# Kernel tuning notes

Measured on AMD Instinct MI355X. Metric: run time of the kernel, lower is better.

## Reference

```python
import jax, jax.numpy as jnp
import numpy as np

NUM_HEADS = 12


def setup_inputs() -> dict:
    key = jax.random.key(0)
    k1, k2, k3, k4 = jax.random.split(key, 4)
    B, N, C = 8, 1024, 768
    x = jax.random.normal(k1, (B, N, C), dtype=jnp.float32)
    # nn.Linear(dim, 3*dim, bias=False): weight applied as x @ W, shape [C, 3C]
    w_qkv = jax.random.normal(k2, (C, 3 * C), dtype=jnp.float32) * (C ** -0.5)
    # nn.Linear(dim, dim) with bias
    w_proj = jax.random.normal(k3, (C, C), dtype=jnp.float32) * (C ** -0.5)
    b_proj = jax.random.normal(k4, (C,), dtype=jnp.float32) * 0.01
    return {"x": x, "w_qkv": w_qkv, "w_proj": w_proj, "b_proj": b_proj, "H": 32, "W": 32}


def reference(x, w_qkv, w_proj, b_proj, H, W):
    B, N, C = x.shape
    nh = NUM_HEADS
    hd = C // nh
    scale = hd ** -0.5
    qkv = (x @ w_qkv).reshape(B, N, 3, nh, hd)
    q, k, v = jnp.moveaxis(qkv, 2, 0)  # each [B, N, nh, hd]
    attn = jnp.einsum("bnhd,bmhd->bhnm", q, k) * scale  # [B, nh, N, N]
    attn = jax.nn.softmax(attn, axis=-1)
    out = jnp.einsum("bhnm,bmhd->bnhd", attn, v).reshape(B, N, C)
    return out @ w_proj + b_proj
```

## Files before the change

kernel.cpp:

```cpp
#include <hip/hip_runtime.h>

typedef __bf16 bf16x8 __attribute__((ext_vector_type(8)));
typedef float f32x4 __attribute__((ext_vector_type(4)));
typedef unsigned short u16;
typedef unsigned int u32;
typedef u16 u16x4 __attribute__((ext_vector_type(4)));

__device__ __forceinline__ u16 f2bf(float f) {
    union { float f; u32 u; } x{f};
    u32 r = x.u + 0x7FFFu + ((x.u >> 16) & 1u);
    return (u16)(r >> 16);
}

__device__ __forceinline__ float ex2(float x) {
#if __has_builtin(__builtin_amdgcn_exp2f)
    return __builtin_amdgcn_exp2f(x);
#else
    return __expf(x * 0.6931471805599453f);
#endif
}

#define GLD16(g, l)                                                            \
    __builtin_amdgcn_global_load_lds(                                          \
        (const __attribute__((address_space(1))) u32*)(g),                     \
        (__attribute__((address_space(3))) u32*)(l), 16, 0, 0)

__global__ void convert_bf16(const float* __restrict__ src, u16* __restrict__ dst, int n4) {
    int i = blockIdx.x * blockDim.x + threadIdx.x;
    if (i < n4) {
        float4 f = *(const float4*)(src + (size_t)i * 4);
        u16x4 u = { f2bf(f.x), f2bf(f.y), f2bf(f.z), f2bf(f.w) };
        *(u16x4*)(dst + (size_t)i * 4) = u;
    }
}

__global__ void transpose_conv(const float* __restrict__ src, u16* __restrict__ dst, int R, int C) {
    __shared__ u16 tile[32][33];
    int bx = blockIdx.x * 32;
    int by = blockIdx.y * 32;
    int x = threadIdx.x, y = threadIdx.y;
    #pragma unroll
    for (int i = 0; i < 32; i += 8)
        tile[y + i][x] = f2bf(src[(size_t)(by + y + i) * C + bx + x]);
    __syncthreads();
    #pragma unroll
    for (int i = 0; i < 32; i += 8)
        dst[(size_t)(bx + y + i) * R + by + x] = tile[x][y + i];
}

__global__ void transpose_v(const u16* __restrict__ qkv, u16* __restrict__ Vt) {
    __shared__ u16 tile[32][33];
    int nb = blockIdx.x * 32, db = blockIdx.y * 32, bh = blockIdx.z;
    int b = bh / 12, h = bh % 12;
    int x = threadIdx.x, y = threadIdx.y;
    #pragma unroll
    for (int i = 0; i < 32; i += 8)
        tile[y + i][x] = qkv[(size_t)(b * 1024 + nb + y + i) * 2304 + 1536 + h * 64 + db + x];
    __syncthreads();
    #pragma unroll
    for (int i = 0; i < 32; i += 8)
        Vt[((size_t)bh * 64 + db + y + i) * 1024 + nb + x] = tile[x][y + i];
}

#define BK 32
template <bool WRITE_BF16, bool ADD_BIAS>
__global__ __launch_bounds__(256) void gemm_bt(
    const u16* __restrict__ A,
    const u16* __restrict__ Bt,
    void* __restrict__ Cp,
    const float* __restrict__ bias,
    int M, int N, int K, int qcols, float qscale)
{
    __shared__ __align__(16) u16 As[128 * BK];
    __shared__ __align__(16) u16 Bs[128 * BK];

    int tid = threadIdx.x;
    int wave = tid >> 6, lane = tid & 63;
    int quad = lane >> 4, l16 = lane & 15;
    int wm = (wave >> 1) * 64, wn = (wave & 1) * 64;
    int bm = blockIdx.y * 128, bn = blockIdx.x * 128;

    f32x4 acc[4][4] = {};

    int srow = lane >> 2;
    int scg = (lane & 3) * 8;
    const u16* Aptr = A + (size_t)(bm + wave * 32 + srow) * K + scg;
    const u16* Bptr = Bt + (size_t)(bn + wave * 32 + srow) * K + scg;
    u16* AsW0 = &As[(wave * 32) * BK];
    u16* AsW1 = &As[(wave * 32 + 16) * BK];
    u16* BsW0 = &Bs[(wave * 32) * BK];
    u16* BsW1 = &Bs[(wave * 32 + 16) * BK];
    const size_t rstepA = (size_t)16 * K;

    for (int k0 = 0; k0 < K; k0 += BK) {
        GLD16(Aptr + k0,          AsW0);
        GLD16(Aptr + k0 + rstepA, AsW1);
        GLD16(Bptr + k0,          BsW0);
        GLD16(Bptr + k0 + rstepA, BsW1);
        __syncthreads();

        bf16x8 af[4], bfr[4];
        #pragma unroll
        for (int i = 0; i < 4; i++) {
            af[i]  = *(const bf16x8*)&As[(wm + i * 16 + l16) * BK + quad * 8];
            bfr[i] = *(const bf16x8*)&Bs[(wn + i * 16 + l16) * BK + quad * 8];
        }
        #pragma unroll
        for (int mi = 0; mi < 4; mi++)
            #pragma unroll
            for (int ni = 0; ni < 4; ni++)
                acc[mi][ni] = __builtin_amdgcn_mfma_f32_16x16x32_bf16(af[mi], bfr[ni], acc[mi][ni], 0, 0, 0);
        __syncthreads();
    }

    #pragma unroll
    for (int mi = 0; mi < 4; mi++) {
        #pragma unroll
        for (int ni = 0; ni < 4; ni++) {
            #pragma unroll
            for (int rg = 0; rg < 4; rg++) {
                int row = bm + wm + mi * 16 + quad * 4 + rg;
                int col = bn + wn + ni * 16 + l16;
                float v = acc[mi][ni][rg];
                if constexpr (WRITE_BF16) {
                    float sc = (col < qcols) ? qscale : 1.0f;
                    ((u16*)Cp)[(size_t)row * N + col] = f2bf(v * sc);
                } else {
                    float bv = ADD_BIAS ? bias[col] : 0.0f;
                    ((float*)Cp)[(size_t)row * N + col] = v + bv;
                }
            }
        }
    }
}

__global__ __launch_bounds__(256, 4) void attn_kernel(
    const u16* __restrict__ qkv,
    const u16* __restrict__ Vt,
    u16* __restrict__ ctx)
{
    __shared__ __align__(16) u16 Ks[2][4096];
    __shared__ __align__(16) u16 Vs[2][4096];
    __shared__ __align__(16) u16 Ps[4096];

    int qt = blockIdx.x;
    int bh = blockIdx.y;
    int b = bh / 12, h = bh % 12;
    int tid = threadIdx.x;
    int wave = tid >> 6, lane = tid & 63;
    int quad = lane >> 4, l16 = lane & 15;

    int sw8 = (quad ^ (l16 & 7)) * 8;

    int qrow = qt * 64 + wave * 16 + l16;
    const u16* qbase = qkv + (size_t)(b * 1024 + qrow) * 2304 + h * 64;
    bf16x8 qf0 = *(const bf16x8*)(qbase + quad * 8);
    bf16x8 qf1 = *(const bf16x8*)(qbase + 32 + quad * 8);

    int srow = lane >> 3;
    int scol = (lane & 7) ^ srow;
    const u16* kA = qkv + (size_t)(b * 1024 + wave * 16 + srow) * 2304 + 768 + h * 64 + scol * 8;
    const u16* vA = Vt + ((size_t)bh * 64 + wave * 16 + srow) * 1024 + scol * 8;

    bf16x8 ones;
    #pragma unroll
    for (int j = 0; j < 8; j++) ((u16*)&ones)[j] = 0x3F80;

    f32x4 o[4] = {};
    f32x4 lsum = {};

    {
        GLD16(kA,            &Ks[0][(wave * 2 + 0) * 512]);
        GLD16(kA + 8 * 2304, &Ks[0][(wave * 2 + 1) * 512]);
        GLD16(vA,            &Vs[0][(wave * 2 + 0) * 512]);
        GLD16(vA + 8 * 1024, &Vs[0][(wave * 2 + 1) * 512]);
    }

    #pragma unroll 2
    for (int kt = 0; kt < 16; kt++) {
        int buf = kt & 1;
        __syncthreads();

        if (kt < 15) {
            const u16* k0 = kA + (size_t)(kt + 1) * (64 * 2304);
            const u16* v0 = vA + (size_t)(kt + 1) * 64;
            GLD16(k0,            &Ks[buf ^ 1][(wave * 2 + 0) * 512]);
            GLD16(k0 + 8 * 2304, &Ks[buf ^ 1][(wave * 2 + 1) * 512]);
            GLD16(v0,            &Vs[buf ^ 1][(wave * 2 + 0) * 512]);
            GLD16(v0 + 8 * 1024, &Vs[buf ^ 1][(wave * 2 + 1) * 512]);
        }

        f32x4 s[4];
        #pragma unroll
        for (int nb = 0; nb < 4; nb++) {
            int rbase = (nb * 16 + l16) * 64;
            bf16x8 kf0 = *(const bf16x8*)&Ks[buf][rbase + sw8];
            bf16x8 kf1 = *(const bf16x8*)&Ks[buf][rbase + (sw8 ^ 32)];
            f32x4 z = {};
            z = __builtin_amdgcn_mfma_f32_16x16x32_bf16(qf0, kf0, z, 0, 0, 0);
            z = __builtin_amdgcn_mfma_f32_16x16x32_bf16(qf1, kf1, z, 0, 0, 0);
            s[nb] = z;
        }

        #pragma unroll
        for (int nb = 0; nb < 4; nb++) {
            #pragma unroll
            for (int rg = 0; rg < 4; rg++) {
                float p = ex2(s[nb][rg]);
                union { float f; u32 u; } c{p};
                u16 pb = (u16)((c.u + 0x8000u) >> 16);
                int row = quad * 4 + rg;
                int cgr = (nb * 2 + (l16 >> 3)) ^ (row & 7);
                Ps[wave * 1024 + row * 64 + cgr * 8 + (l16 & 7)] = pb;
            }
        }
        asm volatile("s_waitcnt lgkmcnt(0)" ::: "memory");

        bf16x8 pf0 = *(const bf16x8*)&Ps[wave * 1024 + l16 * 64 + sw8];
        bf16x8 pf1 = *(const bf16x8*)&Ps[wave * 1024 + l16 * 64 + (sw8 ^ 32)];

        lsum = __builtin_amdgcn_mfma_f32_16x16x32_bf16(pf0, ones, lsum, 0, 0, 0);
        lsum = __builtin_amdgcn_mfma_f32_16x16x32_bf16(pf1, ones, lsum, 0, 0, 0);

        #pragma unroll
        for (int db = 0; db < 4; db++) {
            int rbase = (db * 16 + l16) * 64;
            bf16x8 vf0 = *(const bf16x8*)&Vs[buf][rbase + sw8];
            bf16x8 vf1 = *(const bf16x8*)&Vs[buf][rbase + (sw8 ^ 32)];
            o[db] = __builtin_amdgcn_mfma_f32_16x16x32_bf16(pf0, vf0, o[db], 0, 0, 0);
            o[db] = __builtin_amdgcn_mfma_f32_16x16x32_bf16(pf1, vf1, o[db], 0, 0, 0);
        }
    }

    float rl[4];
    #pragma unroll
    for (int rg = 0; rg < 4; rg++) rl[rg] = 1.0f / lsum[rg];
    #pragma unroll
    for (int db = 0; db < 4; db++) {
        #pragma unroll
        for (int rg = 0; rg < 4; rg++) {
            int row = qt * 64 + wave * 16 + quad * 4 + rg;
            int col = h * 64 + db * 16 + l16;
            ctx[(size_t)(b * 1024 + row) * 768 + col] = f2bf(o[db][rg] * rl[rg]);
        }
    }
}

extern "C" void kernel_launch(void* const* d_in, const int* in_sizes, int n_in,
                              void* d_out, int out_size, void* d_ws, size_t ws_size,
                              hipStream_t stream) {
    const float* x      = (const float*)d_in[0];
    const float* w_qkv  = (const float*)d_in[1];
    const float* w_proj = (const float*)d_in[2];
    const float* b_proj = (const float*)d_in[3];
    float* out = (float*)d_out;

    const int BN = 8192;
    const int C = 768, C3 = 2304;
    const float CE = 0.18033688011112042f;

    u16* Xb      = (u16*)d_ws;
    u16* Wqkv_t  = Xb + (size_t)BN * C;
    u16* Wproj_t = Wqkv_t + (size_t)C3 * C;
    u16* QKV     = Wproj_t + (size_t)C * C;
    u16* Vt      = QKV + (size_t)BN * C3;
    u16* Ctx     = Vt + (size_t)96 * 64 * 1024;

    convert_bf16<<<(BN * C / 4 + 255) / 256, 256, 0, stream>>>(x, Xb, BN * C / 4);
    transpose_conv<<<dim3(C3 / 32, C / 32), dim3(32, 8), 0, stream>>>(w_qkv, Wqkv_t, C, C3);
    transpose_conv<<<dim3(C / 32, C / 32), dim3(32, 8), 0, stream>>>(w_proj, Wproj_t, C, C);

    gemm_bt<true, false><<<dim3(C3 / 128, BN / 128), 256, 0, stream>>>(
        Xb, Wqkv_t, (void*)QKV, nullptr, BN, C3, C, C, CE);

    transpose_v<<<dim3(32, 2, 96), dim3(32, 8), 0, stream>>>(QKV, Vt);

    attn_kernel<<<dim3(16, 96), 256, 0, stream>>>(QKV, Vt, Ctx);

    gemm_bt<false, true><<<dim3(C / 128, BN / 128), 256, 0, stream>>>(
        Ctx, Wproj_t, (void*)out, b_proj, BN, C, C, 0, 1.0f);
}
```

Before: 215.0 us.

## Double-buffer GEMM LDS tiles and widen V transpose to 64x64 tiles

The bf16 GEMM now ping-pongs two LDS buffers and issues the next K-slice's global-to-LDS loads before computing on the current one. This drops one barrier per iteration and overlaps load latency with MFMA work. K becomes a template constant so the loop can unroll, and the V transpose switches to 64x64 tiles with 32-bit accesses. LDS per block doubles, which may lower occupancy.

New measurement: 216.1 us. No clear change (+0.5%).

```diff
diff --git a/kernel.cpp b/kernel.cpp
--- a/kernel.cpp
+++ b/kernel.cpp
@@ -48,31 +48,38 @@
         dst[(size_t)(bx + y + i) * R + by + x] = tile[x][y + i];
 }
 
-__global__ void transpose_v(const u16* __restrict__ qkv, u16* __restrict__ Vt) {
-    __shared__ u16 tile[32][33];
-    int nb = blockIdx.x * 32, db = blockIdx.y * 32, bh = blockIdx.z;
+__global__ __launch_bounds__(256) void transpose_v(const u16* __restrict__ qkv, u16* __restrict__ Vt) {
+    __shared__ u16 tile[64][66];
+    int nb = blockIdx.x * 64, bh = blockIdx.y;
     int b = bh / 12, h = bh % 12;
-    int x = threadIdx.x, y = threadIdx.y;
-    #pragma unroll
-    for (int i = 0; i < 32; i += 8)
-        tile[y + i][x] = qkv[(size_t)(b * 1024 + nb + y + i) * 2304 + 1536 + h * 64 + db + x];
+    int tid = threadIdx.x;
+    int rn = tid >> 5, d2 = tid & 31;
+    #pragma unroll
+    for (int i = 0; i < 8; i++) {
+        const u16* src = qkv + (size_t)(b * 1024 + nb + i * 8 + rn) * 2304 + 1536 + h * 64 + d2 * 2;
+        *(u32*)&tile[i * 8 + rn][d2 * 2] = *(const u32*)src;
+    }
     __syncthreads();
-    #pragma unroll
-    for (int i = 0; i < 32; i += 8)
-        Vt[((size_t)bh * 64 + db + y + i) * 1024 + nb + x] = tile[x][y + i];
+    int rd = tid >> 5, n2 = tid & 31;
+    #pragma unroll
+    for (int i = 0; i < 8; i++) {
+        int d = i * 8 + rd;
+        u32 v = (u32)tile[n2 * 2][d] | ((u32)tile[n2 * 2 + 1][d] << 16);
+        *(u32*)&Vt[((size_t)bh * 64 + d) * 1024 + nb + n2 * 2] = v;
+    }
 }
 
 #define BK 32
-template <bool WRITE_BF16, bool ADD_BIAS>
+template <bool WRITE_BF16, bool ADD_BIAS, int K>
 __global__ __launch_bounds__(256) void gemm_bt(
     const u16* __restrict__ A,
     const u16* __restrict__ Bt,
     void* __restrict__ Cp,
     const float* __restrict__ bias,
-    int M, int N, int K, int qcols, float qscale)
+    int M, int N, int qcols, float qscale)
 {
-    __shared__ __align__(16) u16 As[128 * BK];
-    __shared__ __align__(16) u16 Bs[128 * BK];
+    __shared__ __align__(16) u16 As[2][128 * BK];
+    __shared__ __align__(16) u16 Bs[2][128 * BK];
 
     int tid = threadIdx.x;
     int wave = tid >> 6, lane = tid & 63;
@@ -86,31 +93,41 @@
     int scg = (lane & 3) * 8;
     const u16* Aptr = A + (size_t)(bm + wave * 32 + srow) * K + scg;
     const u16* Bptr = Bt + (size_t)(bn + wave * 32 + srow) * K + scg;
-    u16* AsW0 = &As[(wave * 32) * BK];
-    u16* AsW1 = &As[(wave * 32 + 16) * BK];
-    u16* BsW0 = &Bs[(wave * 32) * BK];
-    u16* BsW1 = &Bs[(wave * 32 + 16) * BK];
-    const size_t rstepA = (size_t)16 * K;
-
-    for (int k0 = 0; k0 < K; k0 += BK) {
-        GLD16(Aptr + k0,          AsW0);
-        GLD16(Aptr + k0 + rstepA, AsW1);
-        GLD16(Bptr + k0,          BsW0);
-        GLD16(Bptr + k0 + rstepA, BsW1);
+    const int w0 = (wave * 32) * BK;
+    const int w1 = (wave * 32 + 16) * BK;
+    const size_t rstep = (size_t)16 * K;
+    constexpr int NIT = K / BK;
+
+    GLD16(Aptr,         &As[0][w0]);
+    GLD16(Aptr + rstep, &As[0][w1]);
+    GLD16(Bptr,         &Bs[0][w0]);
+    GLD16(Bptr + rstep, &Bs[0][w1]);
+
+    #pragma unroll 2
+    for (int it = 0; it < NIT; it++) {
+        int buf = it & 1;
         __syncthreads();
 
+        if (it + 1 < NIT) {
+            const u16* a = Aptr + (it + 1) * BK;
+            const u16* bp = Bptr + (it + 1) * BK;
+            GLD16(a,          &As[buf ^ 1][w0]);
+            GLD16(a + rstep,  &As[buf ^ 1][w1]);
+            GLD16(bp,         &Bs[buf ^ 1][w0]);
+            GLD16(bp + rstep, &Bs[buf ^ 1][w1]);
+        }
+
         bf16x8 af[4], bfr[4];
         #pragma unroll
         for (int i = 0; i < 4; i++) {
-            af[i]  = *(const bf16x8*)&As[(wm + i * 16 + l16) * BK + quad * 8];
-            bfr[i] = *(const bf16x8*)&Bs[(wn + i * 16 + l16) * BK + quad * 8];
+            af[i]  = *(const bf16x8*)&As[buf][(wm + i * 16 + l16) * BK + quad * 8];
+            bfr[i] = *(const bf16x8*)&Bs[buf][(wn + i * 16 + l16) * BK + quad * 8];
         }
         #pragma unroll
         for (int mi = 0; mi < 4; mi++)
             #pragma unroll
             for (int ni = 0; ni < 4; ni++)
                 acc[mi][ni] = __builtin_amdgcn_mfma_f32_16x16x32_bf16(af[mi], bfr[ni], acc[mi][ni], 0, 0, 0);
-        __syncthreads();
     }
 
     #pragma unroll
@@ -270,13 +287,13 @@
     transpose_conv<<<dim3(C3 / 32, C / 32), dim3(32, 8), 0, stream>>>(w_qkv, Wqkv_t, C, C3);
     transpose_conv<<<dim3(C / 32, C / 32), dim3(32, 8), 0, stream>>>(w_proj, Wproj_t, C, C);
 
-    gemm_bt<true, false><<<dim3(C3 / 128, BN / 128), 256, 0, stream>>>(
-        Xb, Wqkv_t, (void*)QKV, nullptr, BN, C3, C, C, CE);
-
-    transpose_v<<<dim3(32, 2, 96), dim3(32, 8), 0, stream>>>(QKV, Vt);
+    gemm_bt<true, false, 768><<<dim3(C3 / 128, BN / 128), 256, 0, stream>>>(
+        Xb, Wqkv_t, (void*)QKV, nullptr, BN, C3, C, CE);
+
+    transpose_v<<<dim3(16, 96), 256, 0, stream>>>(QKV, Vt);
 
     attn_kernel<<<dim3(16, 96), 256, 0, stream>>>(QKV, Vt, Ctx);
 
-    gemm_bt<false, true><<<dim3(C / 128, BN / 128), 256, 0, stream>>>(
-        Ctx, Wproj_t, (void*)out, b_proj, BN, C, C, 0, 1.0f);
-}
+    gemm_bt<false, true, 768><<<dim3(C / 128, BN / 128), 256, 0, stream>>>(
+        Ctx, Wproj_t, (void*)out, b_proj, BN, C, 0, 1.0f);
+}
```

## Fuse input conversion and V transpose into QKV GEMM, merge weight prep kernels

Applied to the files above, without the earlier changes.

The QKV GEMM now reads fp32 activations directly, converts them to bf16 in registers and stores them into padded LDS, which removes the separate convert pass and its bf16 copy of x. For the V column blocks the MFMA operands are swapped so the accumulator comes out transposed, and V is written straight into the transposed layout, dropping the transpose_v kernel. The two weight transpose kernels are merged into a single launch. The trade-off is that the A-tile load becomes synchronous register loads instead of direct-to-LDS loads, and the V writes are narrow 2-byte stores.

After: 248.9 us. 1.16x slower.

```diff
diff --git a/kernel.cpp b/kernel.cpp
--- a/kernel.cpp
+++ b/kernel.cpp
@@ -4,7 +4,7 @@
 typedef float f32x4 __attribute__((ext_vector_type(4)));
 typedef unsigned short u16;
 typedef unsigned int u32;
-typedef u16 u16x4 __attribute__((ext_vector_type(4)));
+typedef u16 u16x8 __attribute__((ext_vector_type(8)));
 
 __device__ __forceinline__ u16 f2bf(float f) {
     union { float f; u32 u; } x{f};
@@ -25,20 +25,16 @@
         (const __attribute__((address_space(1))) u32*)(g),                     \
         (__attribute__((address_space(3))) u32*)(l), 16, 0, 0)
 
-__global__ void convert_bf16(const float* __restrict__ src, u16* __restrict__ dst, int n4) {
-    int i = blockIdx.x * blockDim.x + threadIdx.x;
-    if (i < n4) {
-        float4 f = *(const float4*)(src + (size_t)i * 4);
-        u16x4 u = { f2bf(f.x), f2bf(f.y), f2bf(f.z), f2bf(f.w) };
-        *(u16x4*)(dst + (size_t)i * 4) = u;
-    }
-}
-
-__global__ void transpose_conv(const float* __restrict__ src, u16* __restrict__ dst, int R, int C) {
+__global__ __launch_bounds__(256) void prep_weights(
+    const float* __restrict__ wq, const float* __restrict__ wp,
+    u16* __restrict__ WqT, u16* __restrict__ WpT)
+{
     __shared__ u16 tile[32][33];
-    int bx = blockIdx.x * 32;
-    int by = blockIdx.y * 32;
-    int x = threadIdx.x, y = threadIdx.y;
+    int id = blockIdx.x;
+    const float* src; u16* dst; int R, C, bx, by;
+    if (id < 1728) { src = wq; dst = WqT; R = 768; C = 2304; bx = (id % 72) * 32; by = (id / 72) * 32; }
+    else { id -= 1728; src = wp; dst = WpT; R = 768; C = 768; bx = (id % 24) * 32; by = (id / 24) * 32; }
+    int x = threadIdx.x & 31, y = threadIdx.x >> 5;
     #pragma unroll
     for (int i = 0; i < 32; i += 8)
         tile[y + i][x] = f2bf(src[(size_t)(by + y + i) * C + bx + x]);
@@ -48,62 +44,141 @@
         dst[(size_t)(bx + y + i) * R + by + x] = tile[x][y + i];
 }
 
-__global__ void transpose_v(const u16* __restrict__ qkv, u16* __restrict__ Vt) {
-    __shared__ u16 tile[32][33];
-    int nb = blockIdx.x * 32, db = blockIdx.y * 32, bh = blockIdx.z;
-    int b = bh / 12, h = bh % 12;
-    int x = threadIdx.x, y = threadIdx.y;
-    #pragma unroll
-    for (int i = 0; i < 32; i += 8)
-        tile[y + i][x] = qkv[(size_t)(b * 1024 + nb + y + i) * 2304 + 1536 + h * 64 + db + x];
-    __syncthreads();
-    #pragma unroll
-    for (int i = 0; i < 32; i += 8)
-        Vt[((size_t)bh * 64 + db + y + i) * 1024 + nb + x] = tile[x][y + i];
-}
-
-#define BK 32
-template <bool WRITE_BF16, bool ADD_BIAS>
-__global__ __launch_bounds__(256) void gemm_bt(
-    const u16* __restrict__ A,
-    const u16* __restrict__ Bt,
-    void* __restrict__ Cp,
-    const float* __restrict__ bias,
-    int M, int N, int K, int qcols, float qscale)
+template <int K>
+__global__ __launch_bounds__(256) void gemm_qkv(
+    const float* __restrict__ X,
+    const u16* __restrict__ Wt,
+    u16* __restrict__ QKV,
+    u16* __restrict__ Vt,
+    float qscale)
 {
-    __shared__ __align__(16) u16 As[128 * BK];
-    __shared__ __align__(16) u16 Bs[128 * BK];
+    __shared__ u16 As[128][40];
+    __shared__ __align__(16) u16 Bs[128 * 32];
 
     int tid = threadIdx.x;
     int wave = tid >> 6, lane = tid & 63;
     int quad = lane >> 4, l16 = lane & 15;
     int wm = (wave >> 1) * 64, wn = (wave & 1) * 64;
     int bm = blockIdx.y * 128, bn = blockIdx.x * 128;
+    bool vsec = (bn >= 1536);
 
     f32x4 acc[4][4] = {};
 
-    int srow = lane >> 2;
-    int scg = (lane & 3) * 8;
+    int r = tid >> 1, cgA = (tid & 1) * 16;
+    const float* Ap = X + (size_t)(bm + r) * K + cgA;
+
+    int srow = lane >> 2, scg = (lane & 3) * 8;
+    const u16* Bp = Wt + (size_t)(bn + wave * 32 + srow) * K + scg;
+    const int w0 = (wave * 32) * 32;
+    const int w1 = (wave * 32 + 16) * 32;
+    const size_t rstep = (size_t)16 * K;
+
+    for (int k0 = 0; k0 < K; k0 += 32) {
+        GLD16(Bp + k0,         &Bs[w0]);
+        GLD16(Bp + k0 + rstep, &Bs[w1]);
+        float4 f0 = *(const float4*)(Ap + k0);
+        float4 f1 = *(const float4*)(Ap + k0 + 4);
+        float4 f2 = *(const float4*)(Ap + k0 + 8);
+        float4 f3 = *(const float4*)(Ap + k0 + 12);
+        u16x8 lo = { f2bf(f0.x), f2bf(f0.y), f2bf(f0.z), f2bf(f0.w),
+                     f2bf(f1.x), f2bf(f1.y), f2bf(f1.z), f2bf(f1.w) };
+        u16x8 hi = { f2bf(f2.x), f2bf(f2.y), f2bf(f2.z), f2bf(f2.w),
+                     f2bf(f3.x), f2bf(f3.y), f2bf(f3.z), f2bf(f3.w) };
+        *(u16x8*)&As[r][cgA]     = lo;
+        *(u16x8*)&As[r][cgA + 8] = hi;
+        __syncthreads();
+
+        bf16x8 af[4], bfr[4];
+        #pragma unroll
+        for (int i = 0; i < 4; i++) {
+            af[i]  = *(const bf16x8*)&As[wm + i * 16 + l16][quad * 8];
+            bfr[i] = *(const bf16x8*)&Bs[(wn + i * 16 + l16) * 32 + quad * 8];
+        }
+        if (!vsec) {
+            #pragma unroll
+            for (int mi = 0; mi < 4; mi++)
+                #pragma unroll
+                for (int ni = 0; ni < 4; ni++)
+                    acc[mi][ni] = __builtin_amdgcn_mfma_f32_16x16x32_bf16(af[mi], bfr[ni], acc[mi][ni], 0, 0, 0);
+        } else {
+            #pragma unroll
+            for (int mi = 0; mi < 4; mi++)
+                #pragma unroll
+                for (int ni = 0; ni < 4; ni++)
+                    acc[mi][ni] = __builtin_amdgcn_mfma_f32_16x16x32_bf16(bfr[ni], af[mi], acc[mi][ni], 0, 0, 0);
+        }
+        __syncthreads();
+    }
+
+    if (!vsec) {
+        #pragma unroll
+        for (int mi = 0; mi < 4; mi++) {
+            #pragma unroll
+            for (int ni = 0; ni < 4; ni++) {
+                #pragma unroll
+                for (int rg = 0; rg < 4; rg++) {
+                    int row = bm + wm + mi * 16 + quad * 4 + rg;
+                    int col = bn + wn + ni * 16 + l16;
+                    float sc = (col < 768) ? qscale : 1.0f;
+                    QKV[(size_t)row * 2304 + col] = f2bf(acc[mi][ni][rg] * sc);
+                }
+            }
+        }
+    } else {
+        #pragma unroll
+        for (int mi = 0; mi < 4; mi++) {
+            #pragma unroll
+            for (int ni = 0; ni < 4; ni++) {
+                #pragma unroll
+                for (int rg = 0; rg < 4; rg++) {
+                    int d = (bn - 1536) + wn + ni * 16 + quad * 4 + rg;
+                    int ng = bm + wm + mi * 16 + l16;
+                    int b = ng >> 10, n = ng & 1023, h = d >> 6;
+                    Vt[((size_t)(b * 12 + h) * 64 + (d & 63)) * 1024 + n] = f2bf(acc[mi][ni][rg]);
+                }
+            }
+        }
+    }
+}
+
+template <int K>
+__global__ __launch_bounds__(256) void gemm_proj(
+    const u16* __restrict__ A,
+    const u16* __restrict__ Bt,
+    float* __restrict__ Cp,
+    const float* __restrict__ bias,
+    int M, int N)
+{
+    __shared__ __align__(16) u16 As[128 * 32];
+    __shared__ __align__(16) u16 Bs[128 * 32];
+
+    int tid = threadIdx.x;
+    int wave = tid >> 6, lane = tid & 63;
+    int quad = lane >> 4, l16 = lane & 15;
+    int wm = (wave >> 1) * 64, wn = (wave & 1) * 64;
+    int bm = blockIdx.y * 128, bn = blockIdx.x * 128;
+
+    f32x4 acc[4][4] = {};
+
+    int srow = lane >> 2, scg = (lane & 3) * 8;
     const u16* Aptr = A + (size_t)(bm + wave * 32 + srow) * K + scg;
     const u16* Bptr = Bt + (size_t)(bn + wave * 32 + srow) * K + scg;
-    u16* AsW0 = &As[(wave * 32) * BK];
-    u16* AsW1 = &As[(wave * 32 + 16) * BK];
-    u16* BsW0 = &Bs[(wave * 32) * BK];
-    u16* BsW1 = &Bs[(wave * 32 + 16) * BK];
-    const size_t rstepA = (size_t)16 * K;
-
-    for (int k0 = 0; k0 < K; k0 += BK) {
-        GLD16(Aptr + k0,          AsW0);
-        GLD16(Aptr + k0 + rstepA, AsW1);
-        GLD16(Bptr + k0,          BsW0);
-        GLD16(Bptr + k0 + rstepA, BsW1);
+    const int w0 = (wave * 32) * 32;
+    const int w1 = (wave * 32 + 16) * 32;
+    const size_t rstep = (size_t)16 * K;
+
+    for (int k0 = 0; k0 < K; k0 += 32) {
+        GLD16(Aptr + k0,         &As[w0]);
+        GLD16(Aptr + k0 + rstep, &As[w1]);
+        GLD16(Bptr + k0,         &Bs[w0]);
+        GLD16(Bptr + k0 + rstep, &Bs[w1]);
         __syncthreads();
 
         bf16x8 af[4], bfr[4];
         #pragma unroll
         for (int i = 0; i < 4; i++) {
-            af[i]  = *(const bf16x8*)&As[(wm + i * 16 + l16) * BK + quad * 8];
-            bfr[i] = *(const bf16x8*)&Bs[(wn + i * 16 + l16) * BK + quad * 8];
+            af[i]  = *(const bf16x8*)&As[(wm + i * 16 + l16) * 32 + quad * 8];
+            bfr[i] = *(const bf16x8*)&Bs[(wn + i * 16 + l16) * 32 + quad * 8];
         }
         #pragma unroll
         for (int mi = 0; mi < 4; mi++)
@@ -121,14 +196,7 @@
             for (int rg = 0; rg < 4; rg++) {
                 int row = bm + wm + mi * 16 + quad * 4 + rg;
                 int col = bn + wn + ni * 16 + l16;
-                float v = acc[mi][ni][rg];
-                if constexpr (WRITE_BF16) {
-                    float sc = (col < qcols) ? qscale : 1.0f;
-                    ((u16*)Cp)[(size_t)row * N + col] = f2bf(v * sc);
-                } else {
-                    float bv = ADD_BIAS ? bias[col] : 0.0f;
-                    ((float*)Cp)[(size_t)row * N + col] = v + bv;
-                }
+                Cp[(size_t)row * N + col] = acc[mi][ni][rg] + bias[col];
             }
         }
     }
@@ -259,24 +327,19 @@
     const int C = 768, C3 = 2304;
     const float CE = 0.18033688011112042f;
 
-    u16* Xb      = (u16*)d_ws;
-    u16* Wqkv_t  = Xb + (size_t)BN * C;
+    u16* Wqkv_t  = (u16*)d_ws;
     u16* Wproj_t = Wqkv_t + (size_t)C3 * C;
     u16* QKV     = Wproj_t + (size_t)C * C;
     u16* Vt      = QKV + (size_t)BN * C3;
     u16* Ctx     = Vt + (size_t)96 * 64 * 1024;
 
-    convert_bf16<<<(BN * C / 4 + 255) / 256, 256, 0, stream>>>(x, Xb, BN * C / 4);
-    transpose_conv<<<dim3(C3 / 32, C / 32), dim3(32, 8), 0, stream>>>(w_qkv, Wqkv_t, C, C3);
-    transpose_conv<<<dim3(C / 32, C / 32), dim3(32, 8), 0, stream>>>(w_proj, Wproj_t, C, C);
-
-    gemm_bt<true, false><<<dim3(C3 / 128, BN / 128), 256, 0, stream>>>(
-        Xb, Wqkv_t, (void*)QKV, nullptr, BN, C3, C, C, CE);
-
-    transpose_v<<<dim3(32, 2, 96), dim3(32, 8), 0, stream>>>(QKV, Vt);
+    prep_weights<<<2304, 256, 0, stream>>>(w_qkv, w_proj, Wqkv_t, Wproj_t);
+
+    gemm_qkv<768><<<dim3(C3 / 128, BN / 128), 256, 0, stream>>>(
+        x, Wqkv_t, QKV, Vt, CE);
 
     attn_kernel<<<dim3(16, 96), 256, 0, stream>>>(QKV, Vt, Ctx);
 
-    gemm_bt<false, true><<<dim3(C / 128, BN / 128), 256, 0, stream>>>(
-        Ctx, Wproj_t, (void*)out, b_proj, BN, C, C, 0, 1.0f);
-}
+    gemm_proj<768><<<dim3(C / 128, BN / 128), 256, 0, stream>>>(
+        Ctx, Wproj_t, out, b_proj, BN, C);
+}
```
